# Kernel optimization log

Measured on AMD Instinct MI355X. Metric: run time of the kernel, lower is better.

The kernel has to match this reference:

```python
import jax, jax.numpy as jnp
import numpy as np

N_NODES = 100000
N_EDGES = 1600000
D_IN = 256
D_OUT = 128


def setup_inputs() -> dict:
    key = jax.random.key(0)
    k1, k2, k3, k4, k5, k6 = jax.random.split(key, 6)
    x = jax.random.normal(k1, (N_NODES, D_IN), dtype=jnp.float32)
    edge_src = jax.random.randint(k2, (N_EDGES,), 0, N_NODES, dtype=jnp.int32)
    edge_dst = jax.random.randint(k3, (N_EDGES,), 0, N_NODES, dtype=jnp.int32)
    edge_w = jax.random.uniform(k4, (N_EDGES,), dtype=jnp.float32)
    # GraphConvolution parameters (glorot-style scale)
    W = jax.random.normal(k5, (D_IN, D_OUT), dtype=jnp.float32) / np.sqrt(D_IN)
    b = jax.random.normal(k6, (D_OUT,), dtype=jnp.float32) * 0.01
    return {"x": x, "edge_src": edge_src, "edge_dst": edge_dst,
            "edge_w": edge_w, "W": W, "b": b}


def reference(x, edge_src, edge_dst, edge_w, W, b):
    # GraphConvolution: out = adj @ (x @ W) + b, adj given as weighted edge list
    support = x @ W                                   # [N, D_OUT] dense GEMM
    msgs = support[edge_src] * edge_w[:, None]        # [E, D_OUT] gather + scale
    out = jax.ops.segment_sum(msgs, edge_dst, num_segments=N_NODES)  # scatter-add
    return out + b
```

## Files before the change

### kernel.cpp

```cpp
#include <hip/hip_runtime.h>

#define N_NODES 100000
#define N_EDGES 1600000
#define D_IN 256
#define D_OUT 128

#define NPB 256
#define NB 391
#define REGION 4864
#define CHUNK 4096
#define NCHUNK ((N_EDGES + CHUNK - 1) / CHUNK)

typedef __attribute__((ext_vector_type(8))) short bf16x8;
typedef __attribute__((ext_vector_type(4))) float f32x4;

__device__ __forceinline__ unsigned short f2bf(float f) {
    unsigned u = __float_as_uint(f);
    u += 0x7FFF + ((u >> 16) & 1);
    return (unsigned short)(u >> 16);
}
__device__ __forceinline__ float bflo(unsigned p) { return __uint_as_float(p << 16); }
__device__ __forceinline__ float bfhi(unsigned p) { return __uint_as_float(p & 0xFFFF0000u); }

__global__ void prep_kernel(const float* __restrict__ W,
                            unsigned short* __restrict__ Wt,
                            int* __restrict__ gcursor) {
    int idx = blockIdx.x * 256 + threadIdx.x;
    if (idx < D_OUT * D_IN) {
        int c = idx >> 8;
        int k = idx & 255;
        Wt[idx] = f2bf(W[(size_t)k * D_OUT + c]);
    }
    if (idx < NB) gcursor[idx] = 0;
}

__global__ __launch_bounds__(128) void gemm_mfma_kernel(
        const float* __restrict__ x,
        const unsigned short* __restrict__ Wt,
        unsigned short* __restrict__ supb) {
    __shared__ unsigned short tile[2][16 * 136];
    int wid = (int)((blockIdx.x * blockDim.x + threadIdx.x) >> 6);
    int lane = threadIdx.x & 63;
    int r0 = wid * 16;
    int rowA = r0 + (lane & 15);
    int kgrp = (lane >> 4) * 8;

    f32x4 acc[8];
#pragma unroll
    for (int t = 0; t < 8; ++t) acc[t] = (f32x4){0.f, 0.f, 0.f, 0.f};

    const float* xrow = x + (size_t)rowA * D_IN + kgrp;
    int colbase = lane & 15;

#pragma unroll
    for (int ks = 0; ks < 8; ++ks) {
        int k0 = ks * 32;
        float4 a0 = *(const float4*)(xrow + k0);
        float4 a1 = *(const float4*)(xrow + k0 + 4);
        bf16x8 afrag;
        afrag[0] = (short)f2bf(a0.x); afrag[1] = (short)f2bf(a0.y);
        afrag[2] = (short)f2bf(a0.z); afrag[3] = (short)f2bf(a0.w);
        afrag[4] = (short)f2bf(a1.x); afrag[5] = (short)f2bf(a1.y);
        afrag[6] = (short)f2bf(a1.z); afrag[7] = (short)f2bf(a1.w);
#pragma unroll
        for (int t = 0; t < 8; ++t) {
            bf16x8 bfrag = *(const bf16x8*)(Wt + (size_t)(t * 16 + colbase) * D_IN
                                               + k0 + kgrp);
            acc[t] = __builtin_amdgcn_mfma_f32_16x16x32_bf16(afrag, bfrag,
                                                             acc[t], 0, 0, 0);
        }
    }

    unsigned short* tl = tile[threadIdx.x >> 6];
    int rgrp = (lane >> 4) * 4;
#pragma unroll
    for (int t = 0; t < 8; ++t)
#pragma unroll
        for (int j = 0; j < 4; ++j)
            tl[(rgrp + j) * 136 + t * 16 + colbase] = f2bf(acc[t][j]);
    __syncthreads();

    int row = lane >> 2;
    int c4 = lane & 3;
#pragma unroll
    for (int u = 0; u < 4; ++u) {
        int col0 = u * 32 + c4 * 8;
        int4 v = *(const int4*)(tl + row * 136 + col0);
        *(int4*)(supb + (size_t)(r0 + row) * D_OUT + col0) = v;
    }
}

__global__ __launch_bounds__(512) void binC_kernel(
        const int* __restrict__ src,
        const int* __restrict__ dst,
        const float* __restrict__ ew,
        int* __restrict__ gcursor,
        int2* __restrict__ stg) {
    __shared__ int hist[NB];
    __shared__ int startsh[NB];
    __shared__ int cursor[NB];
    __shared__ int gbase[NB];
    __shared__ int scanbuf[512];
    __shared__ short sbin[CHUNK];
    __shared__ int2 stage[CHUNK];

    int tid = threadIdx.x;
    int e0 = blockIdx.x * CHUNK;
    int cn = N_EDGES - e0;
    if (cn > CHUNK) cn = CHUNK;

    for (int i = tid; i < NB; i += 512) hist[i] = 0;
    __syncthreads();

    int2 tup[8];
    int bin[8];
#pragma unroll
    for (int k = 0; k < 8; ++k) {
        int e = e0 + k * 512 + tid;
        bin[k] = -1;
        if (e < N_EDGES) {
            int d = dst[e];
            bin[k] = d >> 8;
            tup[k] = make_int2(src[e] | ((d & 255) << 17), __float_as_int(ew[e]));
            atomicAdd(&hist[bin[k]], 1);
        }
    }
    __syncthreads();

    int v = (tid < NB) ? hist[tid] : 0;
    scanbuf[tid] = v;
    __syncthreads();
#pragma unroll
    for (int d = 1; d < 512; d <<= 1) {
        int t = (tid >= d) ? scanbuf[tid - d] : 0;
        __syncthreads();
        scanbuf[tid] += t;
        __syncthreads();
    }
    if (tid < NB) {
        startsh[tid] = scanbuf[tid] - v;
        cursor[tid] = scanbuf[tid] - v;
    }
    __syncthreads();

#pragma unroll
    for (int k = 0; k < 8; ++k) {
        if (bin[k] >= 0) {
            int pos = atomicAdd(&cursor[bin[k]], 1);
            stage[pos] = tup[k];
            sbin[pos] = (short)bin[k];
        }
    }

    if (tid < NB && v > 0)
        gbase[tid] = atomicAdd(&gcursor[tid], v);
    __syncthreads();

    for (int i = tid; i < cn; i += 512) {
        int bb = sbin[i];
        int off = gbase[bb] + (i - startsh[bb]);
        if (off < REGION)
            stg[(size_t)bb * REGION + off] = stage[i];
    }
}

__global__ __launch_bounds__(512) void sgather_kernel(
        const unsigned short* __restrict__ supb,
        const int2* __restrict__ stg,
        const int* __restrict__ gcursor,
        const float* __restrict__ b,
        float* __restrict__ out) {
    __shared__ int2 sorted[REGION];
    __shared__ int hist2[256];
    __shared__ int base2[257];
    __shared__ int cur2[256];
    __shared__ int scanbuf[512];

    int tid = threadIdx.x;
    int bkt = blockIdx.x;
    int node0 = bkt * NPB;

    if (tid < 256) hist2[tid] = 0;
    __syncthreads();

    int cnt = gcursor[bkt];
    if (cnt > REGION) cnt = REGION;
    const int2* sg = stg + (size_t)bkt * REGION;

    for (int e = tid; e < cnt; e += 512)
        atomicAdd(&hist2[(sg[e].x >> 17) & 255], 1);
    __syncthreads();

    int v = (tid < 256) ? hist2[tid] : 0;
    scanbuf[tid] = v;
    __syncthreads();
#pragma unroll
    for (int d = 1; d < 512; d <<= 1) {
        int t = (tid >= d) ? scanbuf[tid - d] : 0;
        __syncthreads();
        scanbuf[tid] += t;
        __syncthreads();
    }
    if (tid < 256) {
        base2[tid] = scanbuf[tid] - v;
        cur2[tid] = scanbuf[tid] - v;
    }
    if (tid == 0) base2[256] = cnt;
    __syncthreads();

    for (int e = tid; e < cnt; e += 512) {
        int2 t = sg[e];
        int pos = atomicAdd(&cur2[(t.x >> 17) & 255], 1);
        sorted[pos] = t;
    }
    __syncthreads();

    int wave = tid >> 6, lane = tid & 63;
    float2 bv = ((const float2*)b)[lane];

    for (int jj = 0; jj < 32; ++jj) {
        int j = wave * 32 + jj;
        int node = node0 + j;
        if (node >= N_NODES) break;
        int s = base2[j], t = base2[j + 1];
        float ax = 0.f, ay = 0.f;
        int e = s;
        for (; e + 3 < t; e += 4) {
            int2 t0 = sorted[e];
            int2 t1 = sorted[e + 1];
            int2 t2 = sorted[e + 2];
            int2 t3 = sorted[e + 3];
            unsigned p0 = *(const unsigned*)(supb + (size_t)(t0.x & 0x1FFFF) * D_OUT + 2 * lane);
            unsigned p1 = *(const unsigned*)(supb + (size_t)(t1.x & 0x1FFFF) * D_OUT + 2 * lane);
            unsigned p2 = *(const unsigned*)(supb + (size_t)(t2.x & 0x1FFFF) * D_OUT + 2 * lane);
            unsigned p3 = *(const unsigned*)(supb + (size_t)(t3.x & 0x1FFFF) * D_OUT + 2 * lane);
            float w0 = __int_as_float(t0.y);
            float w1 = __int_as_float(t1.y);
            float w2 = __int_as_float(t2.y);
            float w3 = __int_as_float(t3.y);
            ax += w0 * bflo(p0) + w1 * bflo(p1) + w2 * bflo(p2) + w3 * bflo(p3);
            ay += w0 * bfhi(p0) + w1 * bfhi(p1) + w2 * bfhi(p2) + w3 * bfhi(p3);
        }
        for (; e < t; ++e) {
            int2 t0 = sorted[e];
            unsigned p0 = *(const unsigned*)(supb + (size_t)(t0.x & 0x1FFFF) * D_OUT + 2 * lane);
            float w0 = __int_as_float(t0.y);
            ax += w0 * bflo(p0);
            ay += w0 * bfhi(p0);
        }
        ((float2*)(out + (size_t)node * D_OUT))[lane] =
            make_float2(ax + bv.x, ay + bv.y);
    }
}

extern "C" void kernel_launch(void* const* d_in, const int* in_sizes, int n_in,
                              void* d_out, int out_size, void* d_ws, size_t ws_size,
                              hipStream_t stream) {
    const float* x   = (const float*)d_in[0];
    const int* esrc  = (const int*)d_in[1];
    const int* edst  = (const int*)d_in[2];
    const float* ew  = (const float*)d_in[3];
    const float* W   = (const float*)d_in[4];
    const float* b   = (const float*)d_in[5];
    float* out = (float*)d_out;

    uint8_t* w8 = (uint8_t*)d_ws;
    unsigned short* supb = (unsigned short*)w8;
    int2* stg     = (int2*)(w8 + 25600000);
    int*  gcursor = (int*)(w8 + 40814592);
    unsigned short* Wt = (unsigned short*)(w8 + 40816640);

    prep_kernel<<<(D_OUT * D_IN + 255) / 256, 256, 0, stream>>>(W, Wt, gcursor);

    gemm_mfma_kernel<<<3125, 128, 0, stream>>>(x, Wt, supb);

    binC_kernel<<<NCHUNK, 512, 0, stream>>>(esrc, edst, ew, gcursor, stg);

    sgather_kernel<<<NB, 512, 0, stream>>>(supb, stg, gcursor, b, out);
}
```

Before: 329.8 us.

## Fuse GEMM and edge binning into one launch, halve bucket size to 128 nodes

The dense GEMM and the edge-binning pass now run in one kernel launch, with blocks split by index into bin work and GEMM work, so the two independent stages overlap on the GPU. Buckets now cover 128 nodes instead of 256, doubling the number of gather blocks to improve occupancy and shrink per-block shared memory. The gather kernel also keeps the loaded edge tuples in registers instead of reading global memory twice during the local sort. The changes add a union shared-memory layout and a two-pass scan over 782 bins, and GEMM blocks now use 512 threads with bounds checks for rows past the end.

```diff
diff --git a/kernel.cpp b/kernel.cpp
--- a/kernel.cpp
+++ b/kernel.cpp
@@ -5,11 +5,12 @@
 #define D_IN 256
 #define D_OUT 128
 
-#define NPB 256
-#define NB 391
-#define REGION 4864
+#define NPB 128
+#define NB 782
+#define REGION 2432
 #define CHUNK 4096
-#define NCHUNK ((N_EDGES + CHUNK - 1) / CHUNK)
+#define NCHUNK 391
+#define GEMM_BLOCKS 782
 
 typedef __attribute__((ext_vector_type(8))) short bf16x8;
 typedef __attribute__((ext_vector_type(4))) float f32x4;
@@ -34,133 +35,155 @@
     if (idx < NB) gcursor[idx] = 0;
 }
 
-__global__ __launch_bounds__(128) void gemm_mfma_kernel(
+struct BinSmem {
+    int hist[NB];
+    int startsh[NB];
+    int adj[NB];
+    int scanbuf[512];
+    short sbin[CHUNK];
+    int2 stage[CHUNK];
+};
+struct GemmSmem {
+    unsigned short tile[8][16 * 136];
+};
+union FusedSmem { BinSmem b; GemmSmem g; };
+
+__global__ __launch_bounds__(512) void fused_kernel(
         const float* __restrict__ x,
         const unsigned short* __restrict__ Wt,
-        unsigned short* __restrict__ supb) {
-    __shared__ unsigned short tile[2][16 * 136];
-    int wid = (int)((blockIdx.x * blockDim.x + threadIdx.x) >> 6);
-    int lane = threadIdx.x & 63;
-    int r0 = wid * 16;
-    int rowA = r0 + (lane & 15);
-    int kgrp = (lane >> 4) * 8;
-
-    f32x4 acc[8];
-#pragma unroll
-    for (int t = 0; t < 8; ++t) acc[t] = (f32x4){0.f, 0.f, 0.f, 0.f};
-
-    const float* xrow = x + (size_t)rowA * D_IN + kgrp;
-    int colbase = lane & 15;
-
-#pragma unroll
-    for (int ks = 0; ks < 8; ++ks) {
-        int k0 = ks * 32;
-        float4 a0 = *(const float4*)(xrow + k0);
-        float4 a1 = *(const float4*)(xrow + k0 + 4);
-        bf16x8 afrag;
-        afrag[0] = (short)f2bf(a0.x); afrag[1] = (short)f2bf(a0.y);
-        afrag[2] = (short)f2bf(a0.z); afrag[3] = (short)f2bf(a0.w);
-        afrag[4] = (short)f2bf(a1.x); afrag[5] = (short)f2bf(a1.y);
-        afrag[6] = (short)f2bf(a1.z); afrag[7] = (short)f2bf(a1.w);
-#pragma unroll
-        for (int t = 0; t < 8; ++t) {
-            bf16x8 bfrag = *(const bf16x8*)(Wt + (size_t)(t * 16 + colbase) * D_IN
-                                               + k0 + kgrp);
-            acc[t] = __builtin_amdgcn_mfma_f32_16x16x32_bf16(afrag, bfrag,
-                                                             acc[t], 0, 0, 0);
-        }
-    }
-
-    unsigned short* tl = tile[threadIdx.x >> 6];
-    int rgrp = (lane >> 4) * 4;
-#pragma unroll
-    for (int t = 0; t < 8; ++t)
-#pragma unroll
-        for (int j = 0; j < 4; ++j)
-            tl[(rgrp + j) * 136 + t * 16 + colbase] = f2bf(acc[t][j]);
-    __syncthreads();
-
-    int row = lane >> 2;
-    int c4 = lane & 3;
-#pragma unroll
-    for (int u = 0; u < 4; ++u) {
-        int col0 = u * 32 + c4 * 8;
-        int4 v = *(const int4*)(tl + row * 136 + col0);
-        *(int4*)(supb + (size_t)(r0 + row) * D_OUT + col0) = v;
-    }
-}
-
-__global__ __launch_bounds__(512) void binC_kernel(
+        unsigned short* __restrict__ supb,
         const int* __restrict__ src,
         const int* __restrict__ dst,
         const float* __restrict__ ew,
         int* __restrict__ gcursor,
         int2* __restrict__ stg) {
-    __shared__ int hist[NB];
-    __shared__ int startsh[NB];
-    __shared__ int cursor[NB];
-    __shared__ int gbase[NB];
-    __shared__ int scanbuf[512];
-    __shared__ short sbin[CHUNK];
-    __shared__ int2 stage[CHUNK];
-
+    __shared__ FusedSmem sm;
     int tid = threadIdx.x;
-    int e0 = blockIdx.x * CHUNK;
-    int cn = N_EDGES - e0;
-    if (cn > CHUNK) cn = CHUNK;
-
-    for (int i = tid; i < NB; i += 512) hist[i] = 0;
-    __syncthreads();
-
-    int2 tup[8];
-    int bin[8];
-#pragma unroll
-    for (int k = 0; k < 8; ++k) {
-        int e = e0 + k * 512 + tid;
-        bin[k] = -1;
-        if (e < N_EDGES) {
-            int d = dst[e];
-            bin[k] = d >> 8;
-            tup[k] = make_int2(src[e] | ((d & 255) << 17), __float_as_int(ew[e]));
-            atomicAdd(&hist[bin[k]], 1);
-        }
-    }
-    __syncthreads();
-
-    int v = (tid < NB) ? hist[tid] : 0;
-    scanbuf[tid] = v;
-    __syncthreads();
-#pragma unroll
-    for (int d = 1; d < 512; d <<= 1) {
-        int t = (tid >= d) ? scanbuf[tid - d] : 0;
-        __syncthreads();
-        scanbuf[tid] += t;
-        __syncthreads();
-    }
-    if (tid < NB) {
-        startsh[tid] = scanbuf[tid] - v;
-        cursor[tid] = scanbuf[tid] - v;
-    }
-    __syncthreads();
-
-#pragma unroll
-    for (int k = 0; k < 8; ++k) {
-        if (bin[k] >= 0) {
-            int pos = atomicAdd(&cursor[bin[k]], 1);
-            stage[pos] = tup[k];
-            sbin[pos] = (short)bin[k];
-        }
-    }
-
-    if (tid < NB && v > 0)
-        gbase[tid] = atomicAdd(&gcursor[tid], v);
-    __syncthreads();
-
-    for (int i = tid; i < cn; i += 512) {
-        int bb = sbin[i];
-        int off = gbase[bb] + (i - startsh[bb]);
-        if (off < REGION)
-            stg[(size_t)bb * REGION + off] = stage[i];
+
+    if (blockIdx.x < NCHUNK) {
+        BinSmem& bs = sm.b;
+        int e0 = blockIdx.x * CHUNK;
+        int cn = N_EDGES - e0;
+        if (cn > CHUNK) cn = CHUNK;
+
+        for (int i = tid; i < NB; i += 512) bs.hist[i] = 0;
+        __syncthreads();
+
+        int2 tup[8];
+        int bin[8];
+#pragma unroll
+        for (int k = 0; k < 8; ++k) {
+            int e = e0 + k * 512 + tid;
+            bin[k] = -1;
+            if (e < N_EDGES) {
+                int d = dst[e];
+                bin[k] = d >> 7;
+                tup[k] = make_int2(src[e] | ((d & 127) << 17),
+                                   __float_as_int(ew[e]));
+                atomicAdd(&bs.hist[bin[k]], 1);
+            }
+        }
+        __syncthreads();
+
+        int total0 = 0;
+        for (int half = 0; half < 2; ++half) {
+            int idx = half * 512 + tid;
+            int v = (idx < NB) ? bs.hist[idx] : 0;
+            bs.scanbuf[tid] = v;
+            __syncthreads();
+            for (int d = 1; d < 512; d <<= 1) {
+                int t = (tid >= d) ? bs.scanbuf[tid - d] : 0;
+                __syncthreads();
+                bs.scanbuf[tid] += t;
+                __syncthreads();
+            }
+            if (idx < NB) {
+                int st = total0 + bs.scanbuf[tid] - v;
+                bs.startsh[idx] = st;
+                bs.adj[idx] = st;
+            }
+            total0 += bs.scanbuf[511];
+            __syncthreads();
+        }
+
+#pragma unroll
+        for (int k = 0; k < 8; ++k) {
+            if (bin[k] >= 0) {
+                int pos = atomicAdd(&bs.adj[bin[k]], 1);
+                bs.stage[pos] = tup[k];
+                bs.sbin[pos] = (short)bin[k];
+            }
+        }
+        __syncthreads();
+
+        for (int i = tid; i < NB; i += 512) {
+            int hv = bs.hist[i];
+            if (hv > 0)
+                bs.adj[i] = atomicAdd(&gcursor[i], hv) - bs.startsh[i];
+        }
+        __syncthreads();
+
+        for (int i = tid; i < cn; i += 512) {
+            int bb = bs.sbin[i];
+            int off = bs.adj[bb] + i;
+            if (off < REGION)
+                stg[(size_t)bb * REGION + off] = bs.stage[i];
+        }
+    } else {
+        GemmSmem& gs = sm.g;
+        int gb = blockIdx.x - NCHUNK;
+        int widl = tid >> 6;
+        int lane = tid & 63;
+        int r0 = (gb * 8 + widl) * 16;
+        int rowA = r0 + (lane & 15);
+        int rowAc = rowA < N_NODES ? rowA : N_NODES - 1;
+        int kgrp = (lane >> 4) * 8;
+
+        f32x4 acc[8];
+#pragma unroll
+        for (int t = 0; t < 8; ++t) acc[t] = (f32x4){0.f, 0.f, 0.f, 0.f};
+
+        const float* xrow = x + (size_t)rowAc * D_IN + kgrp;
+        int colbase = lane & 15;
+
+#pragma unroll
+        for (int ks = 0; ks < 8; ++ks) {
+            int k0 = ks * 32;
+            float4 a0 = *(const float4*)(xrow + k0);
+            float4 a1 = *(const float4*)(xrow + k0 + 4);
+            bf16x8 afrag;
+            afrag[0] = (short)f2bf(a0.x); afrag[1] = (short)f2bf(a0.y);
+            afrag[2] = (short)f2bf(a0.z); afrag[3] = (short)f2bf(a0.w);
+            afrag[4] = (short)f2bf(a1.x); afrag[5] = (short)f2bf(a1.y);
+            afrag[6] = (short)f2bf(a1.z); afrag[7] = (short)f2bf(a1.w);
+#pragma unroll
+            for (int t = 0; t < 8; ++t) {
+                bf16x8 bfrag = *(const bf16x8*)(Wt +
+                        (size_t)(t * 16 + colbase) * D_IN + k0 + kgrp);
+                acc[t] = __builtin_amdgcn_mfma_f32_16x16x32_bf16(afrag, bfrag,
+                                                                 acc[t], 0, 0, 0);
+            }
+        }
+
+        unsigned short* tl = gs.tile[widl];
+        int rgrp = (lane >> 4) * 4;
+#pragma unroll
+        for (int t = 0; t < 8; ++t)
+#pragma unroll
+            for (int j = 0; j < 4; ++j)
+                tl[(rgrp + j) * 136 + t * 16 + colbase] = f2bf(acc[t][j]);
+
+        int row = lane >> 2;
+        int c4 = lane & 3;
+        int orow = r0 + row;
+        if (orow < N_NODES) {
+#pragma unroll
+            for (int u = 0; u < 4; ++u) {
+                int col0 = u * 32 + c4 * 8;
+                int4 v = *(const int4*)(tl + row * 136 + col0);
+                *(int4*)(supb + (size_t)orow * D_OUT + col0) = v;
+            }
+        }
     }
 }
 
@@ -171,55 +194,67 @@
         const float* __restrict__ b,
         float* __restrict__ out) {
     __shared__ int2 sorted[REGION];
-    __shared__ int hist2[256];
-    __shared__ int base2[257];
-    __shared__ int cur2[256];
+    __shared__ int hist2[NPB];
+    __shared__ int base2[NPB + 1];
+    __shared__ int cur2[NPB];
     __shared__ int scanbuf[512];
 
     int tid = threadIdx.x;
     int bkt = blockIdx.x;
     int node0 = bkt * NPB;
 
-    if (tid < 256) hist2[tid] = 0;
+    if (tid < NPB) hist2[tid] = 0;
     __syncthreads();
 
     int cnt = gcursor[bkt];
     if (cnt > REGION) cnt = REGION;
     const int2* sg = stg + (size_t)bkt * REGION;
 
-    for (int e = tid; e < cnt; e += 512)
-        atomicAdd(&hist2[(sg[e].x >> 17) & 255], 1);
-    __syncthreads();
-
-    int v = (tid < 256) ? hist2[tid] : 0;
+    int2 tp[5];
+    int dl[5];
+#pragma unroll
+    for (int k = 0; k < 5; ++k) {
+        int e = tid + k * 512;
+        dl[k] = -1;
+        if (e < cnt) {
+            tp[k] = sg[e];
+            dl[k] = (tp[k].x >> 17) & 127;
+            atomicAdd(&hist2[dl[k]], 1);
+        }
+    }
+    __syncthreads();
+
+    int v = (tid < NPB) ? hist2[tid] : 0;
     scanbuf[tid] = v;
     __syncthreads();
-#pragma unroll
-    for (int d = 1; d < 512; d <<= 1) {
+    for (int d = 1; d < NPB; d <<= 1) {
         int t = (tid >= d) ? scanbuf[tid - d] : 0;
         __syncthreads();
         scanbuf[tid] += t;
         __syncthreads();
     }
-    if (tid < 256) {
+    if (tid < NPB) {
         base2[tid] = scanbuf[tid] - v;
         cur2[tid] = scanbuf[tid] - v;
     }
-    if (tid == 0) base2[256] = cnt;
-    __syncthreads();
-
-    for (int e = tid; e < cnt; e += 512) {
-        int2 t = sg[e];
-        int pos = atomicAdd(&cur2[(t.x >> 17) & 255], 1);
-        sorted[pos] = t;
+    if (tid == 0) base2[NPB] = cnt;
+    __syncthreads();
+
+#pragma unroll
+    for (int k = 0; k < 5; ++k) {
+        if (dl[k] >= 0) {
+            int pos = atomicAdd(&cur2[dl[k]], 1);
+            sorted[pos] = tp[k];
+        }
     }
     __syncthreads();
 
     int wave = tid >> 6, lane = tid & 63;
     float2 bv = ((const float2*)b)[lane];
 
-    for (int jj = 0; jj < 32; ++jj) {
-        int j = wave * 32 + jj;
+#pragma unroll 1
+    for (int jj = 0; jj < 16; ++jj) {
+        int j = wave * 16 + jj;
         int node = node0 + j;
         if (node >= N_NODES) break;
         int s = base2[j], t = base2[j + 1];
@@ -268,13 +303,12 @@
     unsigned short* supb = (unsigned short*)w8;
     int2* stg     = (int2*)(w8 + 25600000);
     int*  gcursor = (int*)(w8 + 40814592);
-    unsigned short* Wt = (unsigned short*)(w8 + 40816640);
+    unsigned short* Wt = (unsigned short*)(w8 + 40818688);
 
     prep_kernel<<<(D_OUT * D_IN + 255) / 256, 256, 0, stream>>>(W, Wt, gcursor);
 
-    gemm_mfma_kernel<<<3125, 128, 0, stream>>>(x, Wt, supb);
-
-    binC_kernel<<<NCHUNK, 512, 0, stream>>>(esrc, edst, ew, gcursor, stg);
+    fused_kernel<<<NCHUNK + GEMM_BLOCKS, 512, 0, stream>>>(
+        x, Wt, supb, esrc, edst, ew, gcursor, stg);
 
     sgather_kernel<<<NB, 512, 0, stream>>>(supb, stg, gcursor, b, out);
 }
```

After: 301.8 us. 1.09x faster.
